# Kernel optimization log

Measured on AMD Instinct MI355X. Metric: run time of the kernel, lower is better.

The kernel has to match this reference:

```python
import jax, jax.numpy as jnp
import numpy as np

N_NODES = 50000
N_EDGES = 600000
H = 128
LN_EPS = 1e-5


def _mlp_ln(h, w1, b1, w2, b2, w3, b3, w4, b4, g, be):
    # 4-layer MLP (Linear-ReLU x3, Linear) followed by LayerNorm, as in build_mlp
    h = jax.nn.relu(h @ w1 + b1)
    h = jax.nn.relu(h @ w2 + b2)
    h = jax.nn.relu(h @ w3 + b3)
    h = h @ w4 + b4
    mu = jnp.mean(h, axis=-1, keepdims=True)
    var = jnp.var(h, axis=-1, keepdims=True)
    return (h - mu) * jax.lax.rsqrt(var + LN_EPS) * g + be


def setup_inputs() -> dict:
    key = jax.random.key(0)
    ks = jax.random.split(key, 16)
    s = 0.02
    inp = {
        'x': jax.random.normal(ks[0], (N_NODES, H), jnp.float32),
        'edge_attr': jax.random.normal(ks[1], (N_EDGES, H), jnp.float32),
        'edge_index': jax.random.randint(ks[2], (2, N_EDGES), 0, N_NODES, jnp.int64),
        'e_w1': jax.random.normal(ks[3], (3 * H, H), jnp.float32) * s,
        'e_b1': jnp.zeros((H,), jnp.float32),
        'e_w2': jax.random.normal(ks[4], (H, H), jnp.float32) * s,
        'e_b2': jnp.zeros((H,), jnp.float32),
        'e_w3': jax.random.normal(ks[5], (H, H), jnp.float32) * s,
        'e_b3': jnp.zeros((H,), jnp.float32),
        'e_w4': jax.random.normal(ks[6], (H, H), jnp.float32) * s,
        'e_b4': jnp.zeros((H,), jnp.float32),
        'e_g': jnp.ones((H,), jnp.float32),
        'e_be': jnp.zeros((H,), jnp.float32),
        'n_w1': jax.random.normal(ks[7], (2 * H, H), jnp.float32) * s,
        'n_b1': jnp.zeros((H,), jnp.float32),
        'n_w2': jax.random.normal(ks[8], (H, H), jnp.float32) * s,
        'n_b2': jnp.zeros((H,), jnp.float32),
        'n_w3': jax.random.normal(ks[9], (H, H), jnp.float32) * s,
        'n_b3': jnp.zeros((H,), jnp.float32),
        'n_w4': jax.random.normal(ks[10], (H, H), jnp.float32) * s,
        'n_b4': jnp.zeros((H,), jnp.float32),
        'n_g': jnp.ones((H,), jnp.float32),
        'n_be': jnp.zeros((H,), jnp.float32),
    }
    return inp


def reference(x, edge_attr, edge_index,
              e_w1, e_b1, e_w2, e_b2, e_w3, e_b3, e_w4, e_b4, e_g, e_be,
              n_w1, n_b1, n_w2, n_b2, n_w3, n_b3, n_w4, n_b4, n_g, n_be):
    senders = edge_index[0]
    receivers = edge_index[1]
    # EdgeBlock: gather sender/receiver node features, concat with edge_attr -> MLP+LN
    e_in = jnp.concatenate([x[senders], x[receivers], edge_attr], axis=-1)  # [E, 3H]
    new_edge = _mlp_ln(e_in, e_w1, e_b1, e_w2, e_b2, e_w3, e_b3, e_w4, e_b4, e_g, e_be)
    # NodeBlock: scatter-add updated edge features to receiver nodes, concat with x -> MLP+LN
    agg = jax.ops.segment_sum(new_edge, receivers, num_segments=x.shape[0])  # [N, H]
    n_in = jnp.concatenate([x, agg], axis=-1)  # [N, 2H]
    new_x = _mlp_ln(n_in, n_w1, n_b1, n_w2, n_b2, n_w3, n_b3, n_w4, n_b4, n_g, n_be)
    # Residual adds (GnBlock)
    return (x + new_x, edge_attr + new_edge)
```

## Files before the change

### kernel.cpp

```cpp
#include <hip/hip_runtime.h>

#define N_NODES 50000
#define N_EDGES 600000
#define H 128

typedef __bf16 bf16x8 __attribute__((ext_vector_type(8)));
typedef float f32x4 __attribute__((ext_vector_type(4)));
typedef unsigned short u16;
typedef u16 u16x8 __attribute__((ext_vector_type(8)));
typedef u16 u16x4 __attribute__((ext_vector_type(4)));

#define MW 16384
#define WT_BYTES (11 * MW * 2)
#define XA_OFF WT_BYTES
#define NODE_B (N_NODES * H * 2)
#define XB_OFF (XA_OFF + NODE_B)
#define XN_OFF (XB_OFF + NODE_B)
#define AGG_OFF (XN_OFF + NODE_B)

__device__ inline u16 f2bf(float f) { return __builtin_bit_cast(u16, (__bf16)f); }
__device__ inline float bf2f(u16 u) {
  unsigned v = (unsigned)u << 16;
  return __builtin_bit_cast(float, v);
}

__device__ inline u16x8 cvt8(const float* __restrict__ p) {
  const float4 f0 = ((const float4*)p)[0];
  const float4 f1 = ((const float4*)p)[1];
  u16x8 o;
  o[0] = f2bf(f0.x); o[1] = f2bf(f0.y); o[2] = f2bf(f0.z); o[3] = f2bf(f0.w);
  o[4] = f2bf(f1.x); o[5] = f2bf(f1.y); o[6] = f2bf(f1.z); o[7] = f2bf(f1.w);
  return o;
}

__device__ inline f32x4 mfma_(u16x8 a, u16x8 b, f32x4 c) {
  return __builtin_amdgcn_mfma_f32_16x16x32_bf16(
      __builtin_bit_cast(bf16x8, a), __builtin_bit_cast(bf16x8, b), c, 0, 0, 0);
}


__global__ __launch_bounds__(256) void prep_weights(
    const float* __restrict__ ew1, const float* __restrict__ ew2,
    const float* __restrict__ ew3, const float* __restrict__ ew4,
    const float* __restrict__ nw1, const float* __restrict__ nw2,
    const float* __restrict__ nw3, const float* __restrict__ nw4,
    u16* __restrict__ wt)
{
  const int gid = blockIdx.x * 256 + threadIdx.x;
  if (gid >= 11 * MW) return;
  const int mat = gid >> 14, idx = gid & (MW - 1);
  const int n = idx >> 7, k = idx & 127;
  const float* src; int ro = 0; bool perm = false;
  switch (mat) {
    case 0: src = ew1; ro = 0;   break;
    case 1: src = ew1; ro = 128; break;
    case 2: src = ew1; ro = 256; break;
    case 3: src = ew2; perm = true; break;
    case 4: src = ew3; perm = true; break;
    case 5: src = ew4; perm = true; break;
    case 6: src = nw1; ro = 0;   break;
    case 7: src = nw1; ro = 128; break;
    case 8: src = nw2; perm = true; break;
    case 9: src = nw3; perm = true; break;
    default: src = nw4; perm = true; break;
  }
  int kk = k;
  if (perm) {
    const int k0 = k >> 5, kgg = (k >> 3) & 3, j = k & 7;
    kk = (k0 * 2 + (j >> 2)) * 16 + kgg * 4 + (j & 3);
  }
  wt[gid] = f2bf(src[(ro + kk) * H + n]);
}

template<int NT>
__device__ inline void layerT(const u16* __restrict__ wm,
                              const u16x8 (&bfr)[NT][4],
                              const int la, const int kg,
                              f32x4 (&acc)[NT][8])
{
#pragma unroll
  for (int t = 0; t < NT; ++t)
#pragma unroll
    for (int m = 0; m < 8; ++m) acc[t][m] = {0.f, 0.f, 0.f, 0.f};
#pragma unroll
  for (int k0 = 0; k0 < 4; ++k0) {
#pragma unroll
    for (int m = 0; m < 8; ++m) {
      const u16x8 wf = *(const u16x8*)(wm + (m * 16 + la) * 128 + k0 * 32 + kg * 8);
#pragma unroll
      for (int t = 0; t < NT; ++t)
        acc[t][m] = mfma_(wf, bfr[t][k0], acc[t][m]);
    }
  }
}

template<int NT>
__device__ inline void packT(const f32x4 (&acc)[NT][8],
                             const float* __restrict__ bias,
                             const int kg, u16x8 (&bfr)[NT][4])
{
#pragma unroll
  for (int k0 = 0; k0 < 4; ++k0) {
    const f32x4 bA = *(const f32x4*)(bias + (k0 * 2) * 16 + kg * 4);
    const f32x4 bB = *(const f32x4*)(bias + (k0 * 2 + 1) * 16 + kg * 4);
#pragma unroll
    for (int t = 0; t < NT; ++t) {
      u16x8 o;
#pragma unroll
      for (int j = 0; j < 8; ++j) {
        const int m = k0 * 2 + (j >> 2), r = j & 3;
        float v = acc[t][m][r] + ((j >> 2) ? bB[r] : bA[r]);
        v = v > 0.f ? v : 0.f;
        o[j] = f2bf(v);
      }
      bfr[t][k0] = o;
    }
  }
}

__global__ __launch_bounds__(256) void precompute(
    const float* __restrict__ x, const u16* __restrict__ wt,
    u16* __restrict__ xa, u16* __restrict__ xb, u16* __restrict__ xn)
{
  const int tid = threadIdx.x;
  const int lane = tid & 63, w = tid >> 6;
  const int n0 = blockIdx.x * 64 + w * 16;
  const int la = lane & 15, kg = lane >> 4;
  const int row = n0 + la < N_NODES ? n0 + la : N_NODES - 1;

  u16x8 bfx[1][4];
#pragma unroll
  for (int k0 = 0; k0 < 4; ++k0)
    bfx[0][k0] = cvt8(x + (size_t)row * H + k0 * 32 + kg * 8);

  const int mats[3] = {0, 1, 6};
  u16* outs[3] = {xa, xb, xn};
#pragma unroll
  for (int m3 = 0; m3 < 3; ++m3) {
    f32x4 acc[1][8];
    layerT<1>(wt + mats[m3] * MW, bfx, la, kg, acc);
    if (n0 + la < N_NODES) {
      u16* out = outs[m3] + (size_t)(n0 + la) * H;
#pragma unroll
      for (int m = 0; m < 8; ++m) {
        u16x4 o;
#pragma unroll
        for (int r = 0; r < 4; ++r) o[r] = f2bf(acc[0][m][r]);
        *(u16x4*)(out + (m >> 1) * 32 + kg * 8 + (m & 1) * 4) = o;
      }
    }
  }
}

__global__ __launch_bounds__(256, 4) void edge_kernel(
    const float* __restrict__ ea, const int* __restrict__ eidx,
    const u16* __restrict__ wt,
    const u16* __restrict__ xag, const u16* __restrict__ xbg,
    const float* __restrict__ b1, const float* __restrict__ b2,
    const float* __restrict__ b3, const float* __restrict__ b4,
    const float* __restrict__ g, const float* __restrict__ be,
    float* __restrict__ out2, float* __restrict__ agg)
{
  __shared__ float sT[4][2048];
  const int tid = threadIdx.x;
  const int lane = tid & 63, w = tid >> 6;
  const int e0 = blockIdx.x * 128 + w * 32;
  const int la = lane & 15, kg = lane >> 4;
  const int* __restrict__ snd = eidx;
  const int* __restrict__ rcv = eidx + N_EDGES;
  char* tileB = (char*)sT[w];

  int rA[2];
  rA[0] = e0 + la;      if (rA[0] >= N_EDGES) rA[0] = N_EDGES - 1;
  rA[1] = e0 + 16 + la; if (rA[1] >= N_EDGES) rA[1] = N_EDGES - 1;
  size_t sbH[2], rbH[2];
#pragma unroll
  for (int t = 0; t < 2; ++t) {
    sbH[t] = (size_t)snd[rA[t]] * H;
    rbH[t] = (size_t)rcv[rA[t]] * H;
  }

  u16x8 bfr[2][4];
#pragma unroll
  for (int t = 0; t < 2; ++t)
#pragma unroll
    for (int k0 = 0; k0 < 4; ++k0)
      bfr[t][k0] = cvt8(ea + (size_t)rA[t] * H + k0 * 32 + kg * 8);

  f32x4 acc[2][8];
  layerT<2>(wt + 2 * MW, bfr, la, kg, acc);

  u16x8 xa[2][4], xb[2][4];
#pragma unroll
  for (int t = 0; t < 2; ++t)
#pragma unroll
    for (int k0 = 0; k0 < 4; ++k0) {
      xa[t][k0] = *(const u16x8*)(xag + sbH[t] + k0 * 32 + kg * 8);
      xb[t][k0] = *(const u16x8*)(xbg + rbH[t] + k0 * 32 + kg * 8);
    }

#pragma unroll
  for (int k0 = 0; k0 < 4; ++k0) {
    const f32x4 bA = *(const f32x4*)(b1 + (k0 * 2) * 16 + kg * 4);
    const f32x4 bB = *(const f32x4*)(b1 + (k0 * 2 + 1) * 16 + kg * 4);
#pragma unroll
    for (int t = 0; t < 2; ++t) {
      u16x8 o;
#pragma unroll
      for (int j = 0; j < 8; ++j) {
        const int m = k0 * 2 + (j >> 2), r = j & 3;
        float v = acc[t][m][r] + ((j >> 2) ? bB[r] : bA[r]) +
                  bf2f(xa[t][k0][j]) + bf2f(xb[t][k0][j]);
        v = v > 0.f ? v : 0.f;
        o[j] = f2bf(v);
      }
      bfr[t][k0] = o;
    }
  }

  layerT<2>(wt + 3 * MW, bfr, la, kg, acc);
  packT<2>(acc, b2, kg, bfr);
  layerT<2>(wt + 4 * MW, bfr, la, kg, acc);
  packT<2>(acc, b3, kg, bfr);
  layerT<2>(wt + 5 * MW, bfr, la, kg, acc);

  float vs[2] = {0.f, 0.f}, vq[2] = {0.f, 0.f};
#pragma unroll
  for (int m = 0; m < 8; ++m) {
    const f32x4 b4m = *(const f32x4*)(b4 + m * 16 + kg * 4);
#pragma unroll
    for (int t = 0; t < 2; ++t)
#pragma unroll
      for (int r = 0; r < 4; ++r) {
        const float v = acc[t][m][r] + b4m[r];
        acc[t][m][r] = v;
        vs[t] += v; vq[t] += v * v;
      }
  }
#pragma unroll
  for (int t = 0; t < 2; ++t) {
    vs[t] += __shfl_xor(vs[t], 16, 64);
    vq[t] += __shfl_xor(vq[t], 16, 64);
    vs[t] += __shfl_xor(vs[t], 32, 64);
    vq[t] += __shfl_xor(vq[t], 32, 64);
  }

#pragma unroll
  for (int t = 0; t < 2; ++t) {
    const float mean = vs[t] * (1.0f / 128.0f);
    const float var = vq[t] * (1.0f / 128.0f) - mean * mean;
    const float rstd = rsqrtf(var + 1e-5f);
#pragma unroll
    for (int m = 0; m < 8; ++m) {
      const int co = m * 16 + kg * 4;
      const f32x4 gm = *(const f32x4*)(g + co);
      const f32x4 bem = *(const f32x4*)(be + co);
      f32x4 nv;
#pragma unroll
      for (int r = 0; r < 4; ++r)
        nv[r] = (acc[t][m][r] - mean) * rstd * gm[r] + bem[r];
      const int bc = m * 64 + kg * 16;
      *(f32x4*)(tileB + la * 512 + (bc ^ ((la & 7) << 6))) = nv;
    }
    asm volatile("" ::: "memory");

#pragma unroll
    for (int rr = 0; rr < 4; ++rr) {
      const int trow = kg * 4 + rr;
      const int rowg = e0 + t * 16 + trow;
      if (rowg < N_EDGES) {
        const int rv = rcv[rowg];
        const size_t rb = (size_t)rowg * H;
        float* aggr = agg + (size_t)rv * H;
#pragma unroll
        for (int n = 0; n < 8; ++n) {
          const int col = n * 16 + la;
          const int bc = n * 64 + la * 4;
          const float ne = *(const float*)(tileB + trow * 512 + (bc ^ ((trow & 7) << 6)));
          out2[rb + col] = ea[rb + col] + ne;
          atomicAdd(aggr + col, ne);
        }
      }
    }
    asm volatile("" ::: "memory");
  }
}

__global__ __launch_bounds__(256, 4) void node_kernel(
    const float* __restrict__ x, const float* __restrict__ agg,
    const u16* __restrict__ wt, const u16* __restrict__ xng,
    const float* __restrict__ b1, const float* __restrict__ b2,
    const float* __restrict__ b3, const float* __restrict__ b4,
    const float* __restrict__ g, const float* __restrict__ be,
    float* __restrict__ out1)
{
  const int tid = threadIdx.x;
  const int lane = tid & 63, w = tid >> 6;
  const int n0 = blockIdx.x * 64 + w * 16;
  const int la = lane & 15, kg = lane >> 4;
  const int row = n0 + la < N_NODES ? n0 + la : N_NODES - 1;

  u16x8 bfr[1][4];
#pragma unroll
  for (int k0 = 0; k0 < 4; ++k0)
    bfr[0][k0] = cvt8(agg + (size_t)row * H + k0 * 32 + kg * 8);
  u16x8 xn[4];
#pragma unroll
  for (int k0 = 0; k0 < 4; ++k0)
    xn[k0] = *(const u16x8*)(xng + (size_t)row * H + k0 * 32 + kg * 8);

  f32x4 acc[1][8];
  layerT<1>(wt + 7 * MW, bfr, la, kg, acc);

#pragma unroll
  for (int k0 = 0; k0 < 4; ++k0) {
    const f32x4 bA = *(const f32x4*)(b1 + (k0 * 2) * 16 + kg * 4);
    const f32x4 bB = *(const f32x4*)(b1 + (k0 * 2 + 1) * 16 + kg * 4);
    u16x8 o;
#pragma unroll
    for (int j = 0; j < 8; ++j) {
      const int m = k0 * 2 + (j >> 2), r = j & 3;
      float v = acc[0][m][r] + ((j >> 2) ? bB[r] : bA[r]) + bf2f(xn[k0][j]);
      v = v > 0.f ? v : 0.f;
      o[j] = f2bf(v);
    }
    bfr[0][k0] = o;
  }

  layerT<1>(wt + 8 * MW, bfr, la, kg, acc);
  packT<1>(acc, b2, kg, bfr);
  layerT<1>(wt + 9 * MW, bfr, la, kg, acc);
  packT<1>(acc, b3, kg, bfr);
  layerT<1>(wt + 10 * MW, bfr, la, kg, acc);

  float vs = 0.f, vq = 0.f;
#pragma unroll
  for (int m = 0; m < 8; ++m) {
    const f32x4 b4m = *(const f32x4*)(b4 + m * 16 + kg * 4);
#pragma unroll
    for (int r = 0; r < 4; ++r) {
      const float v = acc[0][m][r] + b4m[r];
      acc[0][m][r] = v;
      vs += v; vq += v * v;
    }
  }
  vs += __shfl_xor(vs, 16, 64);
  vq += __shfl_xor(vq, 16, 64);
  vs += __shfl_xor(vs, 32, 64);
  vq += __shfl_xor(vq, 32, 64);

  if (n0 + la < N_NODES) {
    const float mean = vs * (1.0f / 128.0f);
    const float var = vq * (1.0f / 128.0f) - mean * mean;
    const float rstd = rsqrtf(var + 1e-5f);
    const size_t rb = (size_t)(n0 + la) * H;
#pragma unroll
    for (int m = 0; m < 8; ++m) {
      const int co = m * 16 + kg * 4;
      const f32x4 gm = *(const f32x4*)(g + co);
      const f32x4 bem = *(const f32x4*)(be + co);
      const f32x4 xv = *(const f32x4*)(x + rb + co);
      f32x4 ov;
#pragma unroll
      for (int r = 0; r < 4; ++r)
        ov[r] = xv[r] + (acc[0][m][r] - mean) * rstd * gm[r] + bem[r];
      *(f32x4*)(out1 + rb + co) = ov;
    }
  }
}

extern "C" void kernel_launch(void* const* d_in, const int* in_sizes, int n_in,
                              void* d_out, int out_size, void* d_ws, size_t ws_size,
                              hipStream_t stream) {
  const float* x   = (const float*)d_in[0];
  const float* ea  = (const float*)d_in[1];
  const int*   ei  = (const int*)d_in[2];
  const float* ew1 = (const float*)d_in[3];
  const float* eb1 = (const float*)d_in[4];
  const float* ew2 = (const float*)d_in[5];
  const float* eb2 = (const float*)d_in[6];
  const float* ew3 = (const float*)d_in[7];
  const float* eb3 = (const float*)d_in[8];
  const float* ew4 = (const float*)d_in[9];
  const float* eb4 = (const float*)d_in[10];
  const float* eg  = (const float*)d_in[11];
  const float* ebe = (const float*)d_in[12];
  const float* nw1 = (const float*)d_in[13];
  const float* nb1 = (const float*)d_in[14];
  const float* nw2 = (const float*)d_in[15];
  const float* nb2 = (const float*)d_in[16];
  const float* nw3 = (const float*)d_in[17];
  const float* nb3 = (const float*)d_in[18];
  const float* nw4 = (const float*)d_in[19];
  const float* nb4 = (const float*)d_in[20];
  const float* ng  = (const float*)d_in[21];
  const float* nbe = (const float*)d_in[22];

  char* ws = (char*)d_ws;
  u16* wt = (u16*)ws;
  u16* xa = (u16*)(ws + XA_OFF);
  u16* xb = (u16*)(ws + XB_OFF);
  u16* xn = (u16*)(ws + XN_OFF);
  float* agg = (float*)(ws + AGG_OFF);
  float* out1 = (float*)d_out;
  float* out2 = out1 + (size_t)N_NODES * H;

  hipMemsetAsync(agg, 0, (size_t)N_NODES * H * sizeof(float), stream);
  prep_weights<<<(11 * MW + 255) / 256, 256, 0, stream>>>(
      ew1, ew2, ew3, ew4, nw1, nw2, nw3, nw4, wt);
  precompute<<<(N_NODES + 63) / 64, 256, 0, stream>>>(x, wt, xa, xb, xn);
  edge_kernel<<<(N_EDGES + 127) / 128, 256, 0, stream>>>(
      ea, ei, wt, xa, xb, eb1, eb2, eb3, eb4, eg, ebe, out2, agg);
  node_kernel<<<(N_NODES + 63) / 64, 256, 0, stream>>>(
      x, agg, wt, xn, nb1, nb2, nb3, nb4, ng, nbe, out1);
}
```

Baseline: 862.7 us.

## Store precomputed node projections in fp32 and vectorize edge epilogue

The precomputed per-node first-layer projections (xa, xb, xn) are now stored and gathered as fp32 instead of bf16. The edge and node kernels add them without a bf16 round-trip, which improves accuracy. The edge epilogue now reads the LDS tile, edge_attr and the out2 store as float4 vectors with a new swizzle, and issues four scalar atomics per lane. The asm compiler barriers are replaced by __syncthreads. The trade-off is twice as many bytes in the random per-edge gathers, and atomic address patterns within a wave become strided, which may coalesce less well.

```diff
diff --git a/kernel.cpp b/kernel.cpp
--- a/kernel.cpp
+++ b/kernel.cpp
@@ -8,15 +8,14 @@
 typedef float f32x4 __attribute__((ext_vector_type(4)));
 typedef unsigned short u16;
 typedef u16 u16x8 __attribute__((ext_vector_type(8)));
-typedef u16 u16x4 __attribute__((ext_vector_type(4)));
 
 #define MW 16384
 #define WT_BYTES (11 * MW * 2)
+#define NODE_F (N_NODES * H * 4)
 #define XA_OFF WT_BYTES
-#define NODE_B (N_NODES * H * 2)
-#define XB_OFF (XA_OFF + NODE_B)
-#define XN_OFF (XB_OFF + NODE_B)
-#define AGG_OFF (XN_OFF + NODE_B)
+#define XB_OFF (XA_OFF + NODE_F)
+#define XN_OFF (XB_OFF + NODE_F)
+#define AGG_OFF (XN_OFF + NODE_F)
 
 __device__ inline u16 f2bf(float f) { return __builtin_bit_cast(u16, (__bf16)f); }
 __device__ inline float bf2f(u16 u) {
@@ -120,7 +119,7 @@
 
 __global__ __launch_bounds__(256) void precompute(
     const float* __restrict__ x, const u16* __restrict__ wt,
-    u16* __restrict__ xa, u16* __restrict__ xb, u16* __restrict__ xn)
+    float* __restrict__ xa, float* __restrict__ xb, float* __restrict__ xn)
 {
   const int tid = threadIdx.x;
   const int lane = tid & 63, w = tid >> 6;
@@ -134,20 +133,16 @@
     bfx[0][k0] = cvt8(x + (size_t)row * H + k0 * 32 + kg * 8);
 
   const int mats[3] = {0, 1, 6};
-  u16* outs[3] = {xa, xb, xn};
+  float* outs[3] = {xa, xb, xn};
 #pragma unroll
   for (int m3 = 0; m3 < 3; ++m3) {
     f32x4 acc[1][8];
     layerT<1>(wt + mats[m3] * MW, bfx, la, kg, acc);
     if (n0 + la < N_NODES) {
-      u16* out = outs[m3] + (size_t)(n0 + la) * H;
-#pragma unroll
-      for (int m = 0; m < 8; ++m) {
-        u16x4 o;
-#pragma unroll
-        for (int r = 0; r < 4; ++r) o[r] = f2bf(acc[0][m][r]);
-        *(u16x4*)(out + (m >> 1) * 32 + kg * 8 + (m & 1) * 4) = o;
-      }
+      float* out = outs[m3] + (size_t)(n0 + la) * H;
+#pragma unroll
+      for (int m = 0; m < 8; ++m)
+        *(f32x4*)(out + (m >> 1) * 32 + kg * 8 + (m & 1) * 4) = acc[0][m];
     }
   }
 }
@@ -155,7 +150,7 @@
 __global__ __launch_bounds__(256, 4) void edge_kernel(
     const float* __restrict__ ea, const int* __restrict__ eidx,
     const u16* __restrict__ wt,
-    const u16* __restrict__ xag, const u16* __restrict__ xbg,
+    const float* __restrict__ xag, const float* __restrict__ xbg,
     const float* __restrict__ b1, const float* __restrict__ b2,
     const float* __restrict__ b3, const float* __restrict__ b4,
     const float* __restrict__ g, const float* __restrict__ be,
@@ -190,27 +185,24 @@
   f32x4 acc[2][8];
   layerT<2>(wt + 2 * MW, bfr, la, kg, acc);
 
-  u16x8 xa[2][4], xb[2][4];
-#pragma unroll
-  for (int t = 0; t < 2; ++t)
+#pragma unroll
+  for (int t = 0; t < 2; ++t) {
 #pragma unroll
     for (int k0 = 0; k0 < 4; ++k0) {
-      xa[t][k0] = *(const u16x8*)(xag + sbH[t] + k0 * 32 + kg * 8);
-      xb[t][k0] = *(const u16x8*)(xbg + rbH[t] + k0 * 32 + kg * 8);
-    }
-
-#pragma unroll
-  for (int k0 = 0; k0 < 4; ++k0) {
-    const f32x4 bA = *(const f32x4*)(b1 + (k0 * 2) * 16 + kg * 4);
-    const f32x4 bB = *(const f32x4*)(b1 + (k0 * 2 + 1) * 16 + kg * 4);
-#pragma unroll
-    for (int t = 0; t < 2; ++t) {
+      const int slot = k0 * 32 + kg * 8;
+      const f32x4 a0 = *(const f32x4*)(xag + sbH[t] + slot);
+      const f32x4 a1 = *(const f32x4*)(xag + sbH[t] + slot + 4);
+      const f32x4 c0 = *(const f32x4*)(xbg + rbH[t] + slot);
+      const f32x4 c1 = *(const f32x4*)(xbg + rbH[t] + slot + 4);
+      const f32x4 bA = *(const f32x4*)(b1 + (k0 * 2) * 16 + kg * 4);
+      const f32x4 bB = *(const f32x4*)(b1 + (k0 * 2 + 1) * 16 + kg * 4);
       u16x8 o;
 #pragma unroll
       for (int j = 0; j < 8; ++j) {
         const int m = k0 * 2 + (j >> 2), r = j & 3;
-        float v = acc[t][m][r] + ((j >> 2) ? bB[r] : bA[r]) +
-                  bf2f(xa[t][k0][j]) + bf2f(xb[t][k0][j]);
+        const float xav = (j >> 2) ? a1[r] : a0[r];
+        const float xbv = (j >> 2) ? c1[r] : c0[r];
+        float v = acc[t][m][r] + ((j >> 2) ? bB[r] : bA[r]) + xav + xbv;
         v = v > 0.f ? v : 0.f;
         o[j] = f2bf(v);
       }
@@ -259,10 +251,9 @@
 #pragma unroll
       for (int r = 0; r < 4; ++r)
         nv[r] = (acc[t][m][r] - mean) * rstd * gm[r] + bem[r];
-      const int bc = m * 64 + kg * 16;
-      *(f32x4*)(tileB + la * 512 + (bc ^ ((la & 7) << 6))) = nv;
-    }
-    asm volatile("" ::: "memory");
+      *(f32x4*)(tileB + la * 512 + ((m * 64 + kg * 16) ^ ((la & 7) << 4))) = nv;
+    }
+    __syncthreads();
 
 #pragma unroll
     for (int rr = 0; rr < 4; ++rr) {
@@ -273,22 +264,27 @@
         const size_t rb = (size_t)rowg * H;
         float* aggr = agg + (size_t)rv * H;
 #pragma unroll
-        for (int n = 0; n < 8; ++n) {
-          const int col = n * 16 + la;
-          const int bc = n * 64 + la * 4;
-          const float ne = *(const float*)(tileB + trow * 512 + (bc ^ ((trow & 7) << 6)));
-          out2[rb + col] = ea[rb + col] + ne;
-          atomicAdd(aggr + col, ne);
+        for (int n2 = 0; n2 < 2; ++n2) {
+          const int bc = la * 16 + n2 * 256;
+          const f32x4 nv = *(const f32x4*)(tileB + trow * 512 + (bc ^ ((trow & 7) << 4)));
+          const int col = la * 4 + n2 * 64;
+          const f32x4 ev = *(const f32x4*)(ea + rb + col);
+          f32x4 ov;
+#pragma unroll
+          for (int r = 0; r < 4; ++r) ov[r] = ev[r] + nv[r];
+          *(f32x4*)(out2 + rb + col) = ov;
+#pragma unroll
+          for (int r = 0; r < 4; ++r) atomicAdd(aggr + col + r, nv[r]);
         }
       }
     }
-    asm volatile("" ::: "memory");
+    __syncthreads();
   }
 }
 
 __global__ __launch_bounds__(256, 4) void node_kernel(
     const float* __restrict__ x, const float* __restrict__ agg,
-    const u16* __restrict__ wt, const u16* __restrict__ xng,
+    const u16* __restrict__ wt, const float* __restrict__ xng,
     const float* __restrict__ b1, const float* __restrict__ b2,
     const float* __restrict__ b3, const float* __restrict__ b4,
     const float* __restrict__ g, const float* __restrict__ be,
@@ -304,23 +300,23 @@
 #pragma unroll
   for (int k0 = 0; k0 < 4; ++k0)
     bfr[0][k0] = cvt8(agg + (size_t)row * H + k0 * 32 + kg * 8);
-  u16x8 xn[4];
-#pragma unroll
-  for (int k0 = 0; k0 < 4; ++k0)
-    xn[k0] = *(const u16x8*)(xng + (size_t)row * H + k0 * 32 + kg * 8);
 
   f32x4 acc[1][8];
   layerT<1>(wt + 7 * MW, bfr, la, kg, acc);
 
 #pragma unroll
   for (int k0 = 0; k0 < 4; ++k0) {
+    const int slot = k0 * 32 + kg * 8;
+    const f32x4 a0 = *(const f32x4*)(xng + (size_t)row * H + slot);
+    const f32x4 a1 = *(const f32x4*)(xng + (size_t)row * H + slot + 4);
     const f32x4 bA = *(const f32x4*)(b1 + (k0 * 2) * 16 + kg * 4);
     const f32x4 bB = *(const f32x4*)(b1 + (k0 * 2 + 1) * 16 + kg * 4);
     u16x8 o;
 #pragma unroll
     for (int j = 0; j < 8; ++j) {
       const int m = k0 * 2 + (j >> 2), r = j & 3;
-      float v = acc[0][m][r] + ((j >> 2) ? bB[r] : bA[r]) + bf2f(xn[k0][j]);
+      const float xnv = (j >> 2) ? a1[r] : a0[r];
+      float v = acc[0][m][r] + ((j >> 2) ? bB[r] : bA[r]) + xnv;
       v = v > 0.f ? v : 0.f;
       o[j] = f2bf(v);
     }
@@ -398,9 +394,9 @@
 
   char* ws = (char*)d_ws;
   u16* wt = (u16*)ws;
-  u16* xa = (u16*)(ws + XA_OFF);
-  u16* xb = (u16*)(ws + XB_OFF);
-  u16* xn = (u16*)(ws + XN_OFF);
+  float* xa = (float*)(ws + XA_OFF);
+  float* xb = (float*)(ws + XB_OFF);
+  float* xn = (float*)(ws + XN_OFF);
   float* agg = (float*)(ws + AGG_OFF);
   float* out1 = (float*)d_out;
   float* out2 = out1 + (size_t)N_NODES * H;
```

Result: slower. 1.381 ms (+60.1%).
